# Kernel tuning notes

Hardware: AMD Instinct MI355X
Metric: run time of the kernel (lower is better)

The kernel has to match this reference:

```python
import jax, jax.numpy as jnp
import numpy as np

N, E, DIN, EIN, H, R, G, DEPTH = 50000, 800000, 64, 16, 300, 1024, 256, 5


def setup_inputs() -> dict:
    key = jax.random.key(0)
    ks = jax.random.split(key, 16)
    x = jax.random.normal(ks[0], (N, DIN), jnp.float32)
    edge_attr = jax.random.normal(ks[1], (E, EIN), jnp.float32)
    edge_index = jax.random.randint(ks[2], (2, E), 0, N, dtype=jnp.int32)
    batch = jnp.sort(jax.random.randint(ks[3], (N,), 0, G, dtype=jnp.int32))
    def lin(k, fan_in, shape):
        return jax.random.normal(k, shape, jnp.float32) / np.sqrt(fan_in)
    return {
        "x": x,
        "edge_attr": edge_attr,
        "edge_index": edge_index,
        "batch": batch,
        "W_pn": lin(ks[4], DIN, (DIN, H)),
        "b_pn": jnp.zeros((H,), jnp.float32),
        "W_pe": lin(ks[5], EIN, (EIN, H)),
        "b_pe": jnp.zeros((H,), jnp.float32),
        "W1": lin(ks[6], H, (DEPTH, H, H)),
        "b1": jnp.zeros((DEPTH, H), jnp.float32),
        "W2": lin(ks[7], H, (DEPTH, H, H)),
        "b2": jnp.zeros((DEPTH, H), jnp.float32),
        "W_sp": lin(ks[8], H, (H, R)),
        "b_sp": jnp.zeros((R,), jnp.float32),
        "prelu_a": jnp.float32(0.25),
    }


def reference(x, edge_attr, edge_index, batch, W_pn, b_pn, W_pe, b_pe,
              W1, b1, W2, b2, W_sp, b_sp, prelu_a):
    src = edge_index[0]  # message source (x_j)
    dst = edge_index[1]  # aggregation target
    # input projections
    h = jax.nn.relu(x @ W_pn + b_pn)          # [N, H]
    e = edge_attr @ W_pe + b_pe               # [E, H]
    for i in range(DEPTH):
        # GINEConv: sum_j ReLU(x_j + e_ji), eps = 0
        m = jax.nn.relu(h[src] + e)            # [E, H]
        agg = jax.ops.segment_sum(m, dst, num_segments=N)  # [N, H]
        z = h + agg
        z = jax.nn.relu(z @ W1[i] + b1[i]) @ W2[i] + b2[i]
        h = jax.nn.relu(z) if i < DEPTH - 1 else z
        # dropout is identity in eval mode
    pooled = jax.ops.segment_sum(h, batch, num_segments=G)  # [G, H]
    out = pooled @ W_sp + b_sp                 # [G, R]
    # PReLU with a single learned slope
    return jnp.where(out >= 0, out, prelu_a * out)
```

## Files before the change

### kernel.cpp

```cpp
#include <hip/hip_runtime.h>
#include <hip/hip_bf16.h>

#define N_NODES 50000
#define N_EDGES 800000
#define DIN_    64
#define EIN_    16
#define H_      300
#define R_OUT   1024
#define G_GR    256
#define DEPTH_  5
#define KPAD    320
#define NPAD    50048
#define LDS_S   328

typedef unsigned short ushort_t;
typedef __attribute__((ext_vector_type(8))) short bf16x8;
typedef __attribute__((ext_vector_type(4))) float f32x4;

__device__ __forceinline__ ushort_t f2b(float f) {
  unsigned x = __float_as_uint(f);
  unsigned r = (x + 0x7fffu + ((x >> 16) & 1u)) >> 16;
  return (ushort_t)r;
}
__device__ __forceinline__ float b2f(ushort_t u) {
  return __uint_as_float((unsigned)u << 16);
}

__global__ void pack_weights(const float* __restrict__ W1, const float* __restrict__ W2,
                             ushort_t* __restrict__ Bp1, ushort_t* __restrict__ Bp2) {
  int idx = blockIdx.x * 256 + threadIdx.x;
  const int per = DEPTH_ * 40 * KPAD * 8;
  if (idx >= 2 * per) return;
  const float* W = W1;
  ushort_t* Bp = Bp1;
  int t = idx;
  if (t >= per) { t -= per; W = W2; Bp = Bp2; }
  int j  = t & 7;
  int n  = (t >> 3) % KPAD;
  int kg = ((t >> 3) / KPAD) % 40;
  int i  = t / (40 * KPAD * 8);
  int k  = kg * 8 + j;
  float v = (k < H_ && n < H_) ? W[(i * H_ + k) * H_ + n] : 0.f;
  Bp[t] = f2b(v);
}

__global__ void pack_wpe(const float* __restrict__ Wpe, const float* __restrict__ bpe,
                         ushort_t* __restrict__ Bpe) {
  int t = blockIdx.x * 256 + threadIdx.x;
  if (t >= 4 * KPAD * 8) return;
  int j  = t & 7;
  int n  = (t >> 3) % KPAD;
  int kg = (t >> 3) / KPAD;
  int k  = kg * 8 + j;
  float v = 0.f;
  if (n < H_) {
    if (k < EIN_) v = Wpe[k * H_ + n];
    else if (k == EIN_) v = bpe[n];
  }
  Bpe[t] = f2b(v);
}

__global__ void pack_wpn(const float* __restrict__ Wpn, ushort_t* __restrict__ Bpn) {
  int t = blockIdx.x * 256 + threadIdx.x;
  if (t >= 8 * KPAD * 8) return;
  int j  = t & 7;
  int n  = (t >> 3) % KPAD;
  int kg = (t >> 3) / KPAD;
  int k  = kg * 8 + j;
  float v = (n < H_) ? Wpn[k * H_ + n] : 0.f;
  Bpn[t] = f2b(v);
}

__global__ void hist_deg(const int* __restrict__ dst, int* __restrict__ deg) {
  int e = blockIdx.x * 256 + threadIdx.x;
  if (e < N_EDGES) atomicAdd(deg + dst[e], 1);
}

__global__ __launch_bounds__(1024) void exscan_kernel(const int* __restrict__ deg,
                                                      int* __restrict__ off) {
  __shared__ int wsum[16];
  __shared__ int carry_s;
  int lane = threadIdx.x & 63;
  int wv = threadIdx.x >> 6;
  if (threadIdx.x == 0) carry_s = 0;
  __syncthreads();
  for (int base = 0; base < N_NODES; base += 1024) {
    int i = base + (int)threadIdx.x;
    int orig = (i < N_NODES) ? deg[i] : 0;
    int v = orig;
#pragma unroll
    for (int s = 1; s < 64; s <<= 1) {
      int u = __shfl_up(v, s);
      if (lane >= s) v += u;
    }
    if (lane == 63) wsum[wv] = v;
    __syncthreads();
    if (wv == 0) {
      int t = (lane < 16) ? wsum[lane] : 0;
#pragma unroll
      for (int s = 1; s < 16; s <<= 1) {
        int u = __shfl_up(t, s);
        if (lane >= s) t += u;
      }
      if (lane < 16) wsum[lane] = t;
    }
    __syncthreads();
    int wbase = (wv > 0) ? wsum[wv - 1] : 0;
    if (i < N_NODES) off[i] = carry_s + wbase + v - orig;
    __syncthreads();
    if (threadIdx.x == 1023) carry_s += wsum[15];
    __syncthreads();
  }
  if (threadIdx.x == 0) off[N_NODES] = carry_s;
}

__global__ void scatter_edges(const int* __restrict__ src, const int* __restrict__ dst,
                              int* __restrict__ cursor, int* __restrict__ csr_src,
                              int* __restrict__ csr_eid) {
  int e = blockIdx.x * 256 + threadIdx.x;
  if (e >= N_EDGES) return;
  int d = dst[e];
  int pos = atomicAdd(cursor + d, 1);
  csr_src[pos] = src[e];
  csr_eid[pos] = e;
}

__global__ __launch_bounds__(256) void proj_gemm(const float* __restrict__ x,
                                                 const ushort_t* __restrict__ Bpn,
                                                 const float* __restrict__ bpn,
                                                 ushort_t* __restrict__ hb) {
  int lane = threadIdx.x & 63;
  int wid  = threadIdx.x >> 6;
  int lr = lane & 15, lg = lane >> 4;
  int rowblk  = blockIdx.x * 64 + (wid & 1) * 32;
  int colbase = (wid >> 1) * 160;
  int ar0 = rowblk + lr;       if (ar0 >= N_NODES) ar0 = 0;
  int ar1 = rowblk + 16 + lr;  if (ar1 >= N_NODES) ar1 = 0;
  f32x4 acc[2][10];
#pragma unroll
  for (int a = 0; a < 2; ++a)
#pragma unroll
    for (int c = 0; c < 10; ++c) acc[a][c] = (f32x4){0.f, 0.f, 0.f, 0.f};

#pragma unroll
  for (int ks = 0; ks < 2; ++ks) {
    int k0 = ks * 32;
    const float* xr0 = x + (size_t)ar0 * DIN_ + k0 + lg * 8;
    const float* xr1 = x + (size_t)ar1 * DIN_ + k0 + lg * 8;
    f32x4 l0 = *(const f32x4*)xr0, h0 = *(const f32x4*)(xr0 + 4);
    f32x4 l1 = *(const f32x4*)xr1, h1 = *(const f32x4*)(xr1 + 4);
    bf16x8 a0, a1;
#pragma unroll
    for (int j = 0; j < 4; ++j) {
      a0[j] = (short)f2b(l0[j]); a0[j + 4] = (short)f2b(h0[j]);
      a1[j] = (short)f2b(l1[j]); a1[j + 4] = (short)f2b(h1[j]);
    }
    const ushort_t* bb = Bpn + ((unsigned)(k0 / 8 + lg) * KPAD + colbase + lr) * 8;
#pragma unroll
    for (int c = 0; c < 10; ++c) {
      bf16x8 b = *(const bf16x8*)(bb + c * 16 * 8);
      acc[0][c] = __builtin_amdgcn_mfma_f32_16x16x32_bf16(a0, b, acc[0][c], 0, 0, 0);
      acc[1][c] = __builtin_amdgcn_mfma_f32_16x16x32_bf16(a1, b, acc[1][c], 0, 0, 0);
    }
  }
#pragma unroll
  for (int rt = 0; rt < 2; ++rt) {
#pragma unroll
    for (int c = 0; c < 10; ++c) {
      int col = colbase + c * 16 + lr;
      float bv = (col < H_) ? bpn[col] : 0.f;
#pragma unroll
      for (int r = 0; r < 4; ++r) {
        int row = rowblk + rt * 16 + lg * 4 + r;
        if (row >= N_NODES) continue;
        float v = fmaxf(acc[rt][c][r] + bv, 0.f);
        if (col >= H_) v = 0.f;
        hb[(unsigned)row * KPAD + col] = f2b(v);
      }
    }
  }
}

__global__ __launch_bounds__(320) void node_agg_mfma(const ushort_t* __restrict__ hb,
                                                     const float* __restrict__ ea,
                                                     const ushort_t* __restrict__ Bpe,
                                                     const int* __restrict__ csr_src,
                                                     const int* __restrict__ csr_eid,
                                                     const int* __restrict__ off,
                                                     ushort_t* zb) {
  __shared__ ushort_t lds_e[16 * LDS_S];
  int n = blockIdx.x;
  int tid = threadIdx.x;
  if (n >= N_NODES) {
    zb[(unsigned)n * KPAD + tid] = 0;
    return;
  }
  int lane = tid & 63;
  int w = tid >> 6;
  int lr = lane & 15, lg = lane >> 4;
  int p0 = __builtin_amdgcn_readfirstlane(off[n]);
  int p1 = __builtin_amdgcn_readfirstlane(off[n + 1]);

  bf16x8 bfr[4];
#pragma unroll
  for (int t = 0; t < 4; ++t) {
    int col = w * 64 + t * 16 + lr;
    bfr[t] = *(const bf16x8*)(Bpe + ((unsigned)lg * KPAD + col) * 8);
  }

  float acc = 0.f;
  for (int pc = p0; pc < p1; pc += 16) {
    int cnt = p1 - pc; if (cnt > 16) cnt = 16;
    int eid = csr_eid[pc + lr];
    bf16x8 afr = (bf16x8){0, 0, 0, 0, 0, 0, 0, 0};
    if (lg < 2) {
      const float* ar = ea + (size_t)eid * EIN_ + lg * 8;
      f32x4 lo = *(const f32x4*)ar;
      f32x4 hi = *(const f32x4*)(ar + 4);
#pragma unroll
      for (int j = 0; j < 4; ++j) {
        afr[j] = (short)f2b(lo[j]);
        afr[j + 4] = (short)f2b(hi[j]);
      }
    } else if (lg == 2) {
      afr[0] = (short)0x3F80;
    }
#pragma unroll
    for (int t = 0; t < 4; ++t) {
      f32x4 e4 = __builtin_amdgcn_mfma_f32_16x16x32_bf16(afr, bfr[t], (f32x4){0.f, 0.f, 0.f, 0.f}, 0, 0, 0);
      int col = w * 64 + t * 16 + lr;
#pragma unroll
      for (int r = 0; r < 4; ++r)
        lds_e[(lg * 4 + r) * LDS_S + col] = f2b(e4[r]);
    }
    __syncthreads();
    int e = 0;
    for (; e + 4 <= cnt; e += 4) {
      int s0 = csr_src[pc + e + 0];
      int s1 = csr_src[pc + e + 1];
      int s2 = csr_src[pc + e + 2];
      int s3 = csr_src[pc + e + 3];
      float g0 = b2f(hb[(unsigned)s0 * KPAD + tid]);
      float g1 = b2f(hb[(unsigned)s1 * KPAD + tid]);
      float g2 = b2f(hb[(unsigned)s2 * KPAD + tid]);
      float g3 = b2f(hb[(unsigned)s3 * KPAD + tid]);
      float e0 = b2f(lds_e[(e + 0) * LDS_S + tid]);
      float e1 = b2f(lds_e[(e + 1) * LDS_S + tid]);
      float e2 = b2f(lds_e[(e + 2) * LDS_S + tid]);
      float e3 = b2f(lds_e[(e + 3) * LDS_S + tid]);
      acc += fmaxf(g0 + e0, 0.f);
      acc += fmaxf(g1 + e1, 0.f);
      acc += fmaxf(g2 + e2, 0.f);
      acc += fmaxf(g3 + e3, 0.f);
    }
    for (; e < cnt; ++e) {
      int s = csr_src[pc + e];
      float g = b2f(hb[(unsigned)s * KPAD + tid]);
      float ev = b2f(lds_e[e * LDS_S + tid]);
      acc += fmaxf(g + ev, 0.f);
    }
    __syncthreads();
  }
  unsigned zi = (unsigned)n * KPAD + tid;
  zb[zi] = f2b(b2f(hb[zi]) + acc);
}

template <int RELU_OUT, int OUT_BF16>
__global__ __launch_bounds__(256) void gemm300(const ushort_t* A,
                                               const ushort_t* __restrict__ Bp,
                                               const float* __restrict__ bias,
                                               void* Cout) {
  int lane = threadIdx.x & 63;
  int wid  = threadIdx.x >> 6;
  int lr = lane & 15, lg = lane >> 4;
  int rowblk  = blockIdx.x * 64 + (wid & 1) * 32;
  int colbase = (wid >> 1) * 160;
  f32x4 acc[2][10];
#pragma unroll
  for (int a = 0; a < 2; ++a)
#pragma unroll
    for (int c = 0; c < 10; ++c) acc[a][c] = (f32x4){0.f, 0.f, 0.f, 0.f};

  const ushort_t* Ap = A + (unsigned)(rowblk + lr) * KPAD + lg * 8;
  for (int k0 = 0; k0 < KPAD; k0 += 32) {
    bf16x8 a0 = *(const bf16x8*)(Ap + k0);
    bf16x8 a1 = *(const bf16x8*)(Ap + 16 * KPAD + k0);
    const ushort_t* bb = Bp + ((unsigned)(k0 / 8 + lg) * KPAD + colbase + lr) * 8;
#pragma unroll
    for (int c = 0; c < 10; ++c) {
      bf16x8 b = *(const bf16x8*)(bb + c * 16 * 8);
      acc[0][c] = __builtin_amdgcn_mfma_f32_16x16x32_bf16(a0, b, acc[0][c], 0, 0, 0);
      acc[1][c] = __builtin_amdgcn_mfma_f32_16x16x32_bf16(a1, b, acc[1][c], 0, 0, 0);
    }
  }
  __syncthreads();
#pragma unroll
  for (int rt = 0; rt < 2; ++rt) {
#pragma unroll
    for (int c = 0; c < 10; ++c) {
      int col = colbase + c * 16 + lr;
      float bv = (col < H_) ? bias[col] : 0.f;
#pragma unroll
      for (int r = 0; r < 4; ++r) {
        int row = rowblk + rt * 16 + lg * 4 + r;
        if (row >= N_NODES) continue;
        float v = acc[rt][c][r] + bv;
        if (RELU_OUT) v = fmaxf(v, 0.f);
        if (OUT_BF16) {
          ((ushort_t*)Cout)[(unsigned)row * KPAD + col] = f2b(v);
        } else if (col < H_) {
          ((float*)Cout)[(unsigned)row * H_ + col] = v;
        }
      }
    }
  }
}

__global__ void pool_kernel(const float* __restrict__ h, const int* __restrict__ batch,
                            float* __restrict__ pooled) {
  int g = blockIdx.x;
  int hh = threadIdx.x;
  int lo = 0, hi = N_NODES;
  while (lo < hi) { int mid = (lo + hi) >> 1; if (batch[mid] < g) lo = mid + 1; else hi = mid; }
  int start = lo;
  hi = N_NODES;
  while (lo < hi) { int mid = (lo + hi) >> 1; if (batch[mid] < g + 1) lo = mid + 1; else hi = mid; }
  int end = lo;
  if (hh >= H_) return;
  float s = 0.f;
  for (int n = start; n < end; ++n) s += h[(unsigned)n * H_ + hh];
  pooled[g * H_ + hh] = s;
}

__global__ void final_kernel(const float* __restrict__ pooled, const float* __restrict__ Wsp,
                             const float* __restrict__ bsp, const float* __restrict__ pa,
                             float* __restrict__ out) {
  int f = blockIdx.x * 256 + threadIdx.x;
  if (f >= G_GR * R_OUT) return;
  int g = f >> 10, r = f & 1023;
  float acc = bsp[r];
  const float* pr = pooled + g * H_;
  const float* wc = Wsp + r;
  for (int k = 0; k < H_; ++k) acc += pr[k] * wc[k * R_OUT];
  float a = pa[0];
  out[f] = acc >= 0.f ? acc : a * acc;
}

extern "C" void kernel_launch(void* const* d_in, const int* in_sizes, int n_in,
                              void* d_out, int out_size, void* d_ws, size_t ws_size,
                              hipStream_t stream) {
  const float* x   = (const float*)d_in[0];
  const float* ea  = (const float*)d_in[1];
  const int*   ei  = (const int*)d_in[2];
  const int*   bat = (const int*)d_in[3];
  const float* Wpn = (const float*)d_in[4];
  const float* bpn = (const float*)d_in[5];
  const float* Wpe = (const float*)d_in[6];
  const float* bpe = (const float*)d_in[7];
  const float* W1  = (const float*)d_in[8];
  const float* b1  = (const float*)d_in[9];
  const float* W2  = (const float*)d_in[10];
  const float* b2  = (const float*)d_in[11];
  const float* Wsp = (const float*)d_in[12];
  const float* bsp = (const float*)d_in[13];
  const float* pa  = (const float*)d_in[14];
  const int* src = ei;
  const int* dst = ei + N_EDGES;

  char* ws = (char*)d_ws;
  size_t off_b = 0;
  auto alloc = [&](size_t bytes) {
    void* p = ws + off_b;
    off_b += (bytes + 255) & ~(size_t)255;
    return p;
  };
  ushort_t* hb      = (ushort_t*)alloc(sizeof(ushort_t) * (size_t)NPAD * KPAD);
  ushort_t* zb      = (ushort_t*)alloc(sizeof(ushort_t) * (size_t)NPAD * KPAD);
  float*    h       = (float*)alloc(sizeof(float) * (size_t)N_NODES * H_);
  ushort_t* Bp1     = (ushort_t*)alloc(sizeof(ushort_t) * (size_t)DEPTH_ * 40 * KPAD * 8);
  ushort_t* Bp2     = (ushort_t*)alloc(sizeof(ushort_t) * (size_t)DEPTH_ * 40 * KPAD * 8);
  ushort_t* Bpe     = (ushort_t*)alloc(sizeof(ushort_t) * (size_t)4 * KPAD * 8);
  ushort_t* Bpn     = (ushort_t*)alloc(sizeof(ushort_t) * (size_t)8 * KPAD * 8);
  float*    pooled  = (float*)alloc(sizeof(float) * (size_t)G_GR * H_);
  int*      deg     = (int*)alloc(sizeof(int) * N_NODES);
  int*      offs    = (int*)alloc(sizeof(int) * (N_NODES + 1));
  int*      cursor  = (int*)alloc(sizeof(int) * N_NODES);
  int*      csr_src = (int*)alloc(sizeof(int) * (N_EDGES + 16));
  int*      csr_eid = (int*)alloc(sizeof(int) * (N_EDGES + 16));

  hipMemsetAsync(deg, 0, sizeof(int) * N_NODES, stream);
  hipMemsetAsync(csr_src + N_EDGES, 0, 16 * sizeof(int), stream);
  hipMemsetAsync(csr_eid + N_EDGES, 0, 16 * sizeof(int), stream);
  hist_deg<<<(N_EDGES + 255) / 256, 256, 0, stream>>>(dst, deg);
  exscan_kernel<<<1, 1024, 0, stream>>>(deg, offs);
  hipMemcpyAsync(cursor, offs, sizeof(int) * N_NODES, hipMemcpyDeviceToDevice, stream);
  scatter_edges<<<(N_EDGES + 255) / 256, 256, 0, stream>>>(src, dst, cursor, csr_src, csr_eid);

  pack_weights<<<(2 * DEPTH_ * 40 * KPAD * 8 + 255) / 256, 256, 0, stream>>>(W1, W2, Bp1, Bp2);
  pack_wpe<<<(4 * KPAD * 8 + 255) / 256, 256, 0, stream>>>(Wpe, bpe, Bpe);
  pack_wpn<<<(8 * KPAD * 8 + 255) / 256, 256, 0, stream>>>(Wpn, Bpn);
  proj_gemm<<<NPAD / 64, 256, 0, stream>>>(x, Bpn, bpn, hb);

  for (int i = 0; i < DEPTH_; ++i) {
    node_agg_mfma<<<NPAD, 320, 0, stream>>>(hb, ea, Bpe, csr_src, csr_eid, offs, zb);
    gemm300<1, 1><<<NPAD / 64, 256, 0, stream>>>(zb, Bp1 + (size_t)i * 40 * KPAD * 8, b1 + i * H_, zb);
    if (i < DEPTH_ - 1)
      gemm300<1, 1><<<NPAD / 64, 256, 0, stream>>>(zb, Bp2 + (size_t)i * 40 * KPAD * 8, b2 + i * H_, hb);
    else
      gemm300<0, 0><<<NPAD / 64, 256, 0, stream>>>(zb, Bp2 + (size_t)i * 40 * KPAD * 8, b2 + i * H_, h);
  }

  pool_kernel<<<G_GR, 320, 0, stream>>>(h, bat, pooled);
  final_kernel<<<(G_GR * R_OUT) / 256, 256, 0, stream>>>(pooled, Wsp, bsp, pa, (float*)d_out);
}
```

Baseline: 1.955 ms.

## Double-buffer edge LDS tiles in aggregation and enlarge GEMM row tile

The aggregation kernel now double-buffers the per-chunk edge-embedding tile in LDS. It stores that tile transposed, one slot per column, so each thread reads four edges with a single vector load. Tail edges are padded with bf16 -inf so their ReLU contributes zero without branching, which removes the second barrier per 16-edge chunk. Source indices now come from one coalesced load broadcast with readlane, replacing per-edge scalar loads. Separately, the 300-wide GEMM computes 128 rows per block instead of 64, reusing each B fragment across four A tiles, at the cost of doubled accumulator registers and fewer blocks.

```diff
diff --git a/kernel.cpp b/kernel.cpp
--- a/kernel.cpp
+++ b/kernel.cpp
@@ -11,10 +11,11 @@
 #define DEPTH_  5
 #define KPAD    320
 #define NPAD    50048
-#define LDS_S   328
+#define ESLOT   20
 
 typedef unsigned short ushort_t;
 typedef __attribute__((ext_vector_type(8))) short bf16x8;
+typedef __attribute__((ext_vector_type(4))) short s16x4;
 typedef __attribute__((ext_vector_type(4))) float f32x4;
 
 __device__ __forceinline__ ushort_t f2b(float f) {
@@ -188,7 +189,7 @@
                                                      const int* __restrict__ csr_eid,
                                                      const int* __restrict__ off,
                                                      ushort_t* zb) {
-  __shared__ ushort_t lds_e[16 * LDS_S];
+  __shared__ ushort_t lds_e[2 * KPAD * ESLOT];
   int n = blockIdx.x;
   int tid = threadIdx.x;
   if (n >= N_NODES) {
@@ -200,6 +201,8 @@
   int lr = lane & 15, lg = lane >> 4;
   int p0 = __builtin_amdgcn_readfirstlane(off[n]);
   int p1 = __builtin_amdgcn_readfirstlane(off[n + 1]);
+  unsigned zi = (unsigned)n * KPAD + tid;
+  float self = b2f(hb[zi]);
 
   bf16x8 bfr[4];
 #pragma unroll
@@ -209,8 +212,8 @@
   }
 
   float acc = 0.f;
-  for (int pc = p0; pc < p1; pc += 16) {
-    int cnt = p1 - pc; if (cnt > 16) cnt = 16;
+  int ci = 0;
+  for (int pc = p0; pc < p1; pc += 16, ci ^= 1) {
     int eid = csr_eid[pc + lr];
     bf16x8 afr = (bf16x8){0, 0, 0, 0, 0, 0, 0, 0};
     if (lg < 2) {
@@ -225,44 +228,34 @@
     } else if (lg == 2) {
       afr[0] = (short)0x3F80;
     }
+    int ebase = lg * 4;
+    ushort_t* ldsb = lds_e + ci * (KPAD * ESLOT);
 #pragma unroll
     for (int t = 0; t < 4; ++t) {
       f32x4 e4 = __builtin_amdgcn_mfma_f32_16x16x32_bf16(afr, bfr[t], (f32x4){0.f, 0.f, 0.f, 0.f}, 0, 0, 0);
       int col = w * 64 + t * 16 + lr;
+      s16x4 pk;
 #pragma unroll
       for (int r = 0; r < 4; ++r)
-        lds_e[(lg * 4 + r) * LDS_S + col] = f2b(e4[r]);
-    }
+        pk[r] = (short)((pc + ebase + r < p1) ? f2b(e4[r]) : (ushort_t)0xFF80);
+      *(s16x4*)(ldsb + (unsigned)col * ESLOT + ebase) = pk;
+    }
+    int sv = csr_src[pc + lr];
     __syncthreads();
-    int e = 0;
-    for (; e + 4 <= cnt; e += 4) {
-      int s0 = csr_src[pc + e + 0];
-      int s1 = csr_src[pc + e + 1];
-      int s2 = csr_src[pc + e + 2];
-      int s3 = csr_src[pc + e + 3];
-      float g0 = b2f(hb[(unsigned)s0 * KPAD + tid]);
-      float g1 = b2f(hb[(unsigned)s1 * KPAD + tid]);
-      float g2 = b2f(hb[(unsigned)s2 * KPAD + tid]);
-      float g3 = b2f(hb[(unsigned)s3 * KPAD + tid]);
-      float e0 = b2f(lds_e[(e + 0) * LDS_S + tid]);
-      float e1 = b2f(lds_e[(e + 1) * LDS_S + tid]);
-      float e2 = b2f(lds_e[(e + 2) * LDS_S + tid]);
-      float e3 = b2f(lds_e[(e + 3) * LDS_S + tid]);
-      acc += fmaxf(g0 + e0, 0.f);
-      acc += fmaxf(g1 + e1, 0.f);
-      acc += fmaxf(g2 + e2, 0.f);
-      acc += fmaxf(g3 + e3, 0.f);
-    }
-    for (; e < cnt; ++e) {
-      int s = csr_src[pc + e];
-      float g = b2f(hb[(unsigned)s * KPAD + tid]);
-      float ev = b2f(lds_e[e * LDS_S + tid]);
-      acc += fmaxf(g + ev, 0.f);
-    }
-    __syncthreads();
-  }
-  unsigned zi = (unsigned)n * KPAD + tid;
-  zb[zi] = f2b(b2f(hb[zi]) + acc);
+    const ushort_t* ldsr = lds_e + ci * (KPAD * ESLOT) + (unsigned)tid * ESLOT;
+#pragma unroll
+    for (int eq = 0; eq < 4; ++eq) {
+      if (pc + eq * 4 >= p1) break;
+      s16x4 ep = *(const s16x4*)(ldsr + eq * 4);
+#pragma unroll
+      for (int r = 0; r < 4; ++r) {
+        int s = __builtin_amdgcn_readlane(sv, eq * 4 + r);
+        float g = b2f(hb[(unsigned)s * KPAD + tid]);
+        acc += fmaxf(g + b2f((ushort_t)ep[r]), 0.f);
+      }
+    }
+  }
+  zb[zi] = f2b(self + acc);
 }
 
 template <int RELU_OUT, int OUT_BF16>
@@ -273,11 +266,11 @@
   int lane = threadIdx.x & 63;
   int wid  = threadIdx.x >> 6;
   int lr = lane & 15, lg = lane >> 4;
-  int rowblk  = blockIdx.x * 64 + (wid & 1) * 32;
+  int rowblk  = blockIdx.x * 128 + (wid & 1) * 64;
   int colbase = (wid >> 1) * 160;
-  f32x4 acc[2][10];
-#pragma unroll
-  for (int a = 0; a < 2; ++a)
+  f32x4 acc[4][10];
+#pragma unroll
+  for (int a = 0; a < 4; ++a)
 #pragma unroll
     for (int c = 0; c < 10; ++c) acc[a][c] = (f32x4){0.f, 0.f, 0.f, 0.f};
 
@@ -285,17 +278,21 @@
   for (int k0 = 0; k0 < KPAD; k0 += 32) {
     bf16x8 a0 = *(const bf16x8*)(Ap + k0);
     bf16x8 a1 = *(const bf16x8*)(Ap + 16 * KPAD + k0);
+    bf16x8 a2 = *(const bf16x8*)(Ap + 32 * KPAD + k0);
+    bf16x8 a3 = *(const bf16x8*)(Ap + 48 * KPAD + k0);
     const ushort_t* bb = Bp + ((unsigned)(k0 / 8 + lg) * KPAD + colbase + lr) * 8;
 #pragma unroll
     for (int c = 0; c < 10; ++c) {
       bf16x8 b = *(const bf16x8*)(bb + c * 16 * 8);
       acc[0][c] = __builtin_amdgcn_mfma_f32_16x16x32_bf16(a0, b, acc[0][c], 0, 0, 0);
       acc[1][c] = __builtin_amdgcn_mfma_f32_16x16x32_bf16(a1, b, acc[1][c], 0, 0, 0);
+      acc[2][c] = __builtin_amdgcn_mfma_f32_16x16x32_bf16(a2, b, acc[2][c], 0, 0, 0);
+      acc[3][c] = __builtin_amdgcn_mfma_f32_16x16x32_bf16(a3, b, acc[3][c], 0, 0, 0);
     }
   }
   __syncthreads();
 #pragma unroll
-  for (int rt = 0; rt < 2; ++rt) {
+  for (int rt = 0; rt < 4; ++rt) {
 #pragma unroll
     for (int c = 0; c < 10; ++c) {
       int col = colbase + c * 16 + lr;
@@ -403,11 +400,11 @@
 
   for (int i = 0; i < DEPTH_; ++i) {
     node_agg_mfma<<<NPAD, 320, 0, stream>>>(hb, ea, Bpe, csr_src, csr_eid, offs, zb);
-    gemm300<1, 1><<<NPAD / 64, 256, 0, stream>>>(zb, Bp1 + (size_t)i * 40 * KPAD * 8, b1 + i * H_, zb);
+    gemm300<1, 1><<<NPAD / 128, 256, 0, stream>>>(zb, Bp1 + (size_t)i * 40 * KPAD * 8, b1 + i * H_, zb);
     if (i < DEPTH_ - 1)
-      gemm300<1, 1><<<NPAD / 64, 256, 0, stream>>>(zb, Bp2 + (size_t)i * 40 * KPAD * 8, b2 + i * H_, hb);
+      gemm300<1, 1><<<NPAD / 128, 256, 0, stream>>>(zb, Bp2 + (size_t)i * 40 * KPAD * 8, b2 + i * H_, hb);
     else
-      gemm300<0, 0><<<NPAD / 64, 256, 0, stream>>>(zb, Bp2 + (size_t)i * 40 * KPAD * 8, b2 + i * H_, h);
+      gemm300<0, 0><<<NPAD / 128, 256, 0, stream>>>(zb, Bp2 + (size_t)i * 40 * KPAD * 8, b2 + i * H_, h);
   }
 
   pool_kernel<<<G_GR, 320, 0, stream>>>(h, bat, pooled);
```

After: 2.089 ms. 6.8% more time.
